# Kernel optimization log

Hardware: AMD Instinct MI355X
Metric: run time of the kernel (lower is better)

## Reference

```python
import jax, jax.numpy as jnp
import numpy as np

B, LQ, LK, D = 16, 1024, 4096, 256
SQRT_SCALE_INV = 0.25          # D ** -0.25, so scale = 1/sqrt(D)
HALF_BW = 128 // 2             # stripe_bandwdith // 2
NEG_INF = float('-inf')


def setup_inputs() -> dict:
    key = jax.random.key(0)
    k1, k2, k3, k4 = jax.random.split(key, 4)
    query = jax.random.normal(k1, (B, LQ, D), jnp.float32)
    key_t = jax.random.normal(k2, (B, LK, D), jnp.float32)
    value = jax.random.normal(k3, (B, LK, D), jnp.float32)
    # key lengths in [LK//2, LK]; masked_fill in torch requires max == LK
    key_lengths = jax.random.randint(k4, (B,), LK // 2, LK + 1).astype(jnp.int32)
    key_lengths = key_lengths.at[0].set(LK)
    query_lengths = jnp.full((B,), LQ, dtype=jnp.int32)  # full so no all-masked rows
    mask = jnp.arange(LK)[None, :] < key_lengths[:, None]  # [B, LK] bool, True = valid
    return {"query": query, "key": key_t, "value": value, "mask": mask,
            "query_lengths": query_lengths, "key_lengths": key_lengths}


def _stripe_mask(query_lengths, key_lengths, Lq, Lk):
    # band around line y = x * (key_len / query_len), per sample
    gx = jnp.arange(Lq, dtype=jnp.float32)[None, :, None]   # [1,Lq,1]
    gy = jnp.arange(Lk, dtype=jnp.float32)[None, None, :]   # [1,1,Lk]
    slope = (key_lengths.astype(jnp.float32) /
             query_lengths.astype(jnp.float32))[:, None, None]  # [B,1,1]
    center = gx * slope
    return (gy >= center - HALF_BW) & (gy <= center + HALF_BW)  # [B,Lq,Lk] bool


def reference(query, key, value, mask, query_lengths, key_lengths):
    # scores = (q * s) @ (k * s)^T  ==  (q @ k^T) * s^2
    scores = jnp.einsum('bqd,bkd->bqk', query, key) * (SQRT_SCALE_INV * SQRT_SCALE_INV)
    stripe = _stripe_mask(query_lengths, key_lengths, query.shape[1], key.shape[1])
    full_mask = mask[:, None, :] & stripe                    # padding AND stripe
    scores = jnp.where(full_mask, scores.astype(jnp.float32), NEG_INF)
    weight = jax.nn.softmax(scores, axis=-1).astype(query.dtype)
    # module applies no dropout (p=0) and returns (attn_weight, value)
    return (weight, value)
```

## Files before the change

### kernel.cpp

```cpp
#include <hip/hip_runtime.h>
#include <math.h>

constexpr int B_  = 16;
constexpr int LQ_ = 1024;
constexpr int LK_ = 4096;
constexpr int D_  = 256;
constexpr float HALF_BW_F = 64.0f;
constexpr float SCALE = 0.0625f;

typedef float fx4 __attribute__((ext_vector_type(4)));

constexpr int NB_PAD = 168;
constexpr int ROWS_PER_BLK = 16;
constexpr int NUNIT = (B_ * LQ_) / ROWS_PER_BLK;
constexpr int NXCD = 8;
constexpr int UNIT_PER_XCD = NUNIT / NXCD;

template <int CTRL>
__device__ __forceinline__ float dpp_add(float v) {
    int x = __builtin_amdgcn_update_dpp(0, __float_as_int(v), CTRL, 0xF, 0xF, true);
    return v + __int_as_float(x);
}
__device__ __forceinline__ float dpp_reduce16(float v) {
    v = dpp_add<0x118>(v); v = dpp_add<0x114>(v);
    v = dpp_add<0x112>(v); v = dpp_add<0x111>(v);
    return v;
}

__device__ __forceinline__ float grp16_max(float v) {
    #pragma unroll
    for (int off = 8; off > 0; off >>= 1)
        v = fmaxf(v, __shfl_xor(v, off, 64));
    return v;
}
__device__ __forceinline__ float grp16_sum(float v) {
    #pragma unroll
    for (int off = 8; off > 0; off >>= 1)
        v += __shfl_xor(v, off, 64);
    return v;
}

__global__ __launch_bounds__(256, 2) void stripe_attn_kernel(
    const float* __restrict__ Q, const float* __restrict__ K,
    const float* __restrict__ V,
    const int* __restrict__ qlen, const int* __restrict__ klen,
    float* __restrict__ Wout, float* __restrict__ Vout)
{
    const int Bid  = blockIdx.x;
    const int xcd  = Bid & 7;
    const int type = (Bid >> 3) & 1;
    const int rb   = xcd * UNIT_PER_XCD + (Bid >> 4);
    const int tid  = threadIdx.x;
    const int lane = tid & 63;
    const int wave = tid >> 6;
    const int row0 = rb * ROWS_PER_BLK + wave * 4;
    const int b    = row0 >> 10;
    const int qi0  = row0 & (LQ_ - 1);

    __shared__ float s_sc[4][4 * NB_PAD];

    const int   key_len = klen[b];
    const float slope   = (float)key_len / (float)qlen[b];

    int k_lo[4], k_hi[4];
    #pragma unroll
    for (int r = 0; r < 4; ++r) {
        const float center = (float)(qi0 + r) * slope;
        int lo = (int)ceilf(center - HALF_BW_F); if (lo < 0) lo = 0;
        int hi = (int)floorf(center + HALF_BW_F); if (hi > key_len - 1) hi = key_len - 1;
        k_lo[r] = lo; k_hi[r] = hi;
    }

    if (type == 1) {
        const float* vs = V    + (size_t)row0 * 1024;
        float*       vd = Vout + (size_t)row0 * 1024;
        #pragma unroll
        for (int it = 0; it < 16; ++it) {
            const int o = (it * 64 + lane) * 4;
            fx4 t = __builtin_nontemporal_load((const fx4*)(vs + o));
            __builtin_nontemporal_store(t, (fx4*)(vd + o));
        }
        const fx4 z4 = {0.f, 0.f, 0.f, 0.f};
        #pragma unroll
        for (int r = 0; r < 4; ++r) {
            const int s_lo = k_lo[r] >> 8, s_hi = k_hi[r] >> 8;
            float* base = Wout + (size_t)(row0 + r) * LK_;
            #pragma unroll
            for (int j = 0; j < 16; ++j) {
                if (j < s_lo || j > s_hi)
                    __builtin_nontemporal_store(z4, (fx4*)(base + (j * 64 + lane) * 4));
            }
        }
        return;
    }

    const int g   = lane >> 4;
    const int l   = lane & 15;
    const int lo0 = k_lo[0], hi3 = k_hi[3];

    const float* qbase = Q + ((size_t)b * LQ_ + qi0) * D_;
    float4 q0[4], q1[4], q2[4], q3[4];
    #pragma unroll
    for (int m = 0; m < 4; ++m) {
        q0[m] = *(const float4*)(qbase + 0 * D_ + l * 16 + m * 4);
        q1[m] = *(const float4*)(qbase + 1 * D_ + l * 16 + m * 4);
        q2[m] = *(const float4*)(qbase + 2 * D_ + l * 16 + m * 4);
        q3[m] = *(const float4*)(qbase + 3 * D_ + l * 16 + m * 4);
    }

    const float* kbase = K + (size_t)b * LK_ * D_;
    float* sw = s_sc[wave];
    #pragma unroll 2
    for (int kk0 = lo0; kk0 <= hi3; kk0 += 8) {
        const int keyA  = kk0 + g;
        const int keyB  = kk0 + g + 4;
        const int keyAc = (keyA <= hi3) ? keyA : hi3;
        const int keyBc = (keyB <= hi3) ? keyB : hi3;
        const float* kpA = kbase + (size_t)keyAc * D_ + l * 16;
        const float* kpB = kbase + (size_t)keyBc * D_ + l * 16;
        float4 kfA[4], kfB[4];
        #pragma unroll
        for (int m = 0; m < 4; ++m) kfA[m] = *(const float4*)(kpA + m * 4);
        #pragma unroll
        for (int m = 0; m < 4; ++m) kfB[m] = *(const float4*)(kpB + m * 4);
        float a0 = 0.f, a1 = 0.f, a2 = 0.f, a3 = 0.f;
        float b0 = 0.f, b1 = 0.f, b2 = 0.f, b3 = 0.f;
        #pragma unroll
        for (int m = 0; m < 4; ++m) {
            a0 += q0[m].x*kfA[m].x + q0[m].y*kfA[m].y + q0[m].z*kfA[m].z + q0[m].w*kfA[m].w;
            a1 += q1[m].x*kfA[m].x + q1[m].y*kfA[m].y + q1[m].z*kfA[m].z + q1[m].w*kfA[m].w;
            a2 += q2[m].x*kfA[m].x + q2[m].y*kfA[m].y + q2[m].z*kfA[m].z + q2[m].w*kfA[m].w;
            a3 += q3[m].x*kfA[m].x + q3[m].y*kfA[m].y + q3[m].z*kfA[m].z + q3[m].w*kfA[m].w;
            b0 += q0[m].x*kfB[m].x + q0[m].y*kfB[m].y + q0[m].z*kfB[m].z + q0[m].w*kfB[m].w;
            b1 += q1[m].x*kfB[m].x + q1[m].y*kfB[m].y + q1[m].z*kfB[m].z + q1[m].w*kfB[m].w;
            b2 += q2[m].x*kfB[m].x + q2[m].y*kfB[m].y + q2[m].z*kfB[m].z + q2[m].w*kfB[m].w;
            b3 += q3[m].x*kfB[m].x + q3[m].y*kfB[m].y + q3[m].z*kfB[m].z + q3[m].w*kfB[m].w;
        }
        a0 = dpp_reduce16(a0); a1 = dpp_reduce16(a1);
        a2 = dpp_reduce16(a2); a3 = dpp_reduce16(a3);
        b0 = dpp_reduce16(b0); b1 = dpp_reduce16(b1);
        b2 = dpp_reduce16(b2); b3 = dpp_reduce16(b3);
        if (l == 15) {
            if (keyA >= k_lo[0] && keyA <= k_hi[0]) sw[0*NB_PAD + keyA - k_lo[0]] = a0 * SCALE;
            if (keyA >= k_lo[1] && keyA <= k_hi[1]) sw[1*NB_PAD + keyA - k_lo[1]] = a1 * SCALE;
            if (keyA >= k_lo[2] && keyA <= k_hi[2]) sw[2*NB_PAD + keyA - k_lo[2]] = a2 * SCALE;
            if (keyA >= k_lo[3] && keyA <= k_hi[3]) sw[3*NB_PAD + keyA - k_lo[3]] = a3 * SCALE;
            if (keyB >= k_lo[0] && keyB <= k_hi[0]) sw[0*NB_PAD + keyB - k_lo[0]] = b0 * SCALE;
            if (keyB >= k_lo[1] && keyB <= k_hi[1]) sw[1*NB_PAD + keyB - k_lo[1]] = b1 * SCALE;
            if (keyB >= k_lo[2] && keyB <= k_hi[2]) sw[2*NB_PAD + keyB - k_lo[2]] = b2 * SCALE;
            if (keyB >= k_lo[3] && keyB <= k_hi[3]) sw[3*NB_PAD + keyB - k_lo[3]] = b3 * SCALE;
        }
    }

    const float center_g = (float)(qi0 + g) * slope;
    int klo_g = (int)ceilf(center_g - HALF_BW_F); if (klo_g < 0) klo_g = 0;
    int khi_g = (int)floorf(center_g + HALF_BW_F); if (khi_g > key_len - 1) khi_g = key_len - 1;
    const int nb_g = khi_g - klo_g + 1;
    float* sg = sw + g * NB_PAD;

    float vj[9];
    #pragma unroll
    for (int j = 0; j < 9; ++j) {
        const int idx = l + j * 16;
        vj[j] = (idx < nb_g) ? sg[idx] : -INFINITY;
    }
    float mx = vj[0];
    #pragma unroll
    for (int j = 1; j < 9; ++j) mx = fmaxf(mx, vj[j]);
    mx = grp16_max(mx);

    float ej[9], ssum = 0.f;
    #pragma unroll
    for (int j = 0; j < 9; ++j) { ej[j] = __expf(vj[j] - mx); ssum += ej[j]; }
    ssum = grp16_sum(ssum);
    const float inv = 1.0f / ssum;
    #pragma unroll
    for (int j = 0; j < 9; ++j)
        sg[l + j * 16] = ej[j] * inv;

    #pragma unroll
    for (int r = 0; r < 4; ++r) {
        const int klo = k_lo[r], khi = k_hi[r];
        const int s_lo = klo >> 8, s_hi = khi >> 8;
        float* base = Wout + (size_t)(row0 + r) * LK_;
        const float* sr = sw + r * NB_PAD;
        for (int j = s_lo; j <= s_hi; ++j) {
            const int c0 = (j * 64 + lane) * 4;
            float w[4] = {0.f, 0.f, 0.f, 0.f};
            if (c0 + 3 >= klo && c0 <= khi) {
                #pragma unroll
                for (int i = 0; i < 4; ++i) {
                    const int c = c0 + i;
                    if (c >= klo && c <= khi) w[i] = sr[c - klo];
                }
            }
            fx4 w4; w4.x = w[0]; w4.y = w[1]; w4.z = w[2]; w4.w = w[3];
            __builtin_nontemporal_store(w4, (fx4*)(base + c0));
        }
    }
}

extern "C" void kernel_launch(void* const* d_in, const int* in_sizes, int n_in,
                              void* d_out, int out_size, void* d_ws, size_t ws_size,
                              hipStream_t stream) {
    const float* Q    = (const float*)d_in[0];
    const float* K    = (const float*)d_in[1];
    const float* V    = (const float*)d_in[2];
    const int*   qlen = (const int*)d_in[4];
    const int*   klen = (const int*)d_in[5];

    float* Wout = (float*)d_out;
    const size_t W_ELEMS = (size_t)B_ * LQ_ * LK_;
    float* Vout = Wout + W_ELEMS;

    stripe_attn_kernel<<<dim3(2 * NUNIT), dim3(256), 0, stream>>>(
        Q, K, V, qlen, klen, Wout, Vout);
}
```

Before: 96.36 us.

## Share K tiles across waves via async global-to-LDS double-buffered staging

Each block now computes the union of the key bands of its 16 rows and streams those K rows into a double-buffered LDS tile with direct global-to-LDS loads. All four waves then read the shared tile instead of each wave loading its own overlapping K rows from global memory. The Q register layout is changed to match the LDS read pattern. This removes redundant K traffic across waves, but adds a block-wide barrier per 16-key chunk and more LDS, and waves spend cycles on chunks outside their own band.

```diff
diff --git a/kernel.cpp b/kernel.cpp
--- a/kernel.cpp
+++ b/kernel.cpp
@@ -15,6 +15,7 @@
 constexpr int NUNIT = (B_ * LQ_) / ROWS_PER_BLK;
 constexpr int NXCD = 8;
 constexpr int UNIT_PER_XCD = NUNIT / NXCD;
+constexpr int CHUNK = 16;
 
 template <int CTRL>
 __device__ __forceinline__ float dpp_add(float v) {
@@ -26,7 +27,6 @@
     v = dpp_add<0x112>(v); v = dpp_add<0x111>(v);
     return v;
 }
-
 __device__ __forceinline__ float grp16_max(float v) {
     #pragma unroll
     for (int off = 8; off > 0; off >>= 1)
@@ -38,6 +38,13 @@
     for (int off = 8; off > 0; off >>= 1)
         v += __shfl_xor(v, off, 64);
     return v;
+}
+
+__device__ __forceinline__ void gload16(const float* g, float* l) {
+    __builtin_amdgcn_global_load_lds(
+        (const __attribute__((address_space(1))) float*)g,
+        (__attribute__((address_space(3))) float*)l,
+        16, 0, 0);
 }
 
 __global__ __launch_bounds__(256, 2) void stripe_attn_kernel(
@@ -57,8 +64,6 @@
     const int b    = row0 >> 10;
     const int qi0  = row0 & (LQ_ - 1);
 
-    __shared__ float s_sc[4][4 * NB_PAD];
-
     const int   key_len = klen[b];
     const float slope   = (float)key_len / (float)qlen[b];
 
@@ -94,62 +99,94 @@
         return;
     }
 
+    __shared__ float kbuf[2][CHUNK * 256];
+    __shared__ float s_sc[4][4 * NB_PAD];
+
     const int g   = lane >> 4;
     const int l   = lane & 15;
     const int lo0 = k_lo[0], hi3 = k_hi[3];
 
-    const float* qbase = Q + ((size_t)b * LQ_ + qi0) * D_;
+    const int qi_blk = (rb * ROWS_PER_BLK) & (LQ_ - 1);
+    int lo_b = (int)ceilf((float)qi_blk * slope - HALF_BW_F);
+    if (lo_b < 0) lo_b = 0;
+    int hi_b = (int)floorf((float)(qi_blk + 15) * slope + HALF_BW_F);
+    if (hi_b > key_len - 1) hi_b = key_len - 1;
+    const int nchunks = (hi_b - lo_b + CHUNK) / CHUNK;
+
+    const float* qbase = Q + ((size_t)b * LQ_ + qi0) * D_ + l * 4;
     float4 q0[4], q1[4], q2[4], q3[4];
     #pragma unroll
     for (int m = 0; m < 4; ++m) {
-        q0[m] = *(const float4*)(qbase + 0 * D_ + l * 16 + m * 4);
-        q1[m] = *(const float4*)(qbase + 1 * D_ + l * 16 + m * 4);
-        q2[m] = *(const float4*)(qbase + 2 * D_ + l * 16 + m * 4);
-        q3[m] = *(const float4*)(qbase + 3 * D_ + l * 16 + m * 4);
+        q0[m] = *(const float4*)(qbase + 0 * D_ + m * 64);
+        q1[m] = *(const float4*)(qbase + 1 * D_ + m * 64);
+        q2[m] = *(const float4*)(qbase + 2 * D_ + m * 64);
+        q3[m] = *(const float4*)(qbase + 3 * D_ + m * 64);
     }
 
     const float* kbase = K + (size_t)b * LK_ * D_;
     float* sw = s_sc[wave];
-    #pragma unroll 2
-    for (int kk0 = lo0; kk0 <= hi3; kk0 += 8) {
-        const int keyA  = kk0 + g;
-        const int keyB  = kk0 + g + 4;
-        const int keyAc = (keyA <= hi3) ? keyA : hi3;
-        const int keyBc = (keyB <= hi3) ? keyB : hi3;
-        const float* kpA = kbase + (size_t)keyAc * D_ + l * 16;
-        const float* kpB = kbase + (size_t)keyBc * D_ + l * 16;
-        float4 kfA[4], kfB[4];
+
+    auto stage = [&](int c, int buf) {
+        const int base_key = lo_b + c * CHUNK + wave * 4;
         #pragma unroll
-        for (int m = 0; m < 4; ++m) kfA[m] = *(const float4*)(kpA + m * 4);
-        #pragma unroll
-        for (int m = 0; m < 4; ++m) kfB[m] = *(const float4*)(kpB + m * 4);
-        float a0 = 0.f, a1 = 0.f, a2 = 0.f, a3 = 0.f;
-        float b0 = 0.f, b1 = 0.f, b2 = 0.f, b3 = 0.f;
-        #pragma unroll
-        for (int m = 0; m < 4; ++m) {
-            a0 += q0[m].x*kfA[m].x + q0[m].y*kfA[m].y + q0[m].z*kfA[m].z + q0[m].w*kfA[m].w;
-            a1 += q1[m].x*kfA[m].x + q1[m].y*kfA[m].y + q1[m].z*kfA[m].z + q1[m].w*kfA[m].w;
-            a2 += q2[m].x*kfA[m].x + q2[m].y*kfA[m].y + q2[m].z*kfA[m].z + q2[m].w*kfA[m].w;
-            a3 += q3[m].x*kfA[m].x + q3[m].y*kfA[m].y + q3[m].z*kfA[m].z + q3[m].w*kfA[m].w;
-            b0 += q0[m].x*kfB[m].x + q0[m].y*kfB[m].y + q0[m].z*kfB[m].z + q0[m].w*kfB[m].w;
-            b1 += q1[m].x*kfB[m].x + q1[m].y*kfB[m].y + q1[m].z*kfB[m].z + q1[m].w*kfB[m].w;
-            b2 += q2[m].x*kfB[m].x + q2[m].y*kfB[m].y + q2[m].z*kfB[m].z + q2[m].w*kfB[m].w;
-            b3 += q3[m].x*kfB[m].x + q3[m].y*kfB[m].y + q3[m].z*kfB[m].z + q3[m].w*kfB[m].w;
-        }
-        a0 = dpp_reduce16(a0); a1 = dpp_reduce16(a1);
-        a2 = dpp_reduce16(a2); a3 = dpp_reduce16(a3);
-        b0 = dpp_reduce16(b0); b1 = dpp_reduce16(b1);
-        b2 = dpp_reduce16(b2); b3 = dpp_reduce16(b3);
-        if (l == 15) {
-            if (keyA >= k_lo[0] && keyA <= k_hi[0]) sw[0*NB_PAD + keyA - k_lo[0]] = a0 * SCALE;
-            if (keyA >= k_lo[1] && keyA <= k_hi[1]) sw[1*NB_PAD + keyA - k_lo[1]] = a1 * SCALE;
-            if (keyA >= k_lo[2] && keyA <= k_hi[2]) sw[2*NB_PAD + keyA - k_lo[2]] = a2 * SCALE;
-            if (keyA >= k_lo[3] && keyA <= k_hi[3]) sw[3*NB_PAD + keyA - k_lo[3]] = a3 * SCALE;
-            if (keyB >= k_lo[0] && keyB <= k_hi[0]) sw[0*NB_PAD + keyB - k_lo[0]] = b0 * SCALE;
-            if (keyB >= k_lo[1] && keyB <= k_hi[1]) sw[1*NB_PAD + keyB - k_lo[1]] = b1 * SCALE;
-            if (keyB >= k_lo[2] && keyB <= k_hi[2]) sw[2*NB_PAD + keyB - k_lo[2]] = b2 * SCALE;
-            if (keyB >= k_lo[3] && keyB <= k_hi[3]) sw[3*NB_PAD + keyB - k_lo[3]] = b3 * SCALE;
-        }
+        for (int s = 0; s < 4; ++s) {
+            int key = base_key + s;
+            if (key > hi_b) key = hi_b;
+            gload16(kbase + (size_t)key * D_ + lane * 4,
+                    &kbuf[buf][(wave * 4 + s) * 256]);
+        }
+    };
+
+    stage(0, 0);
+    __syncthreads();
+
+    for (int c = 0; c < nchunks; ++c) {
+        const int cb = c & 1;
+        if (c + 1 < nchunks) stage(c + 1, cb ^ 1);
+
+        const int cbase = lo_b + c * CHUNK;
+        if (cbase + CHUNK - 1 >= lo0 && cbase <= hi3) {
+            const float* kl = kbuf[cb];
+            #pragma unroll
+            for (int t = 0; t < 2; ++t) {
+                const int jA = g + 8 * t, jB = g + 4 + 8 * t;
+                const int keyA = cbase + jA, keyB = cbase + jB;
+                float4 kfA[4], kfB[4];
+                #pragma unroll
+                for (int m = 0; m < 4; ++m) {
+                    kfA[m] = *(const float4*)(kl + jA * 256 + m * 64 + l * 4);
+                    kfB[m] = *(const float4*)(kl + jB * 256 + m * 64 + l * 4);
+                }
+                float a0 = 0.f, a1 = 0.f, a2 = 0.f, a3 = 0.f;
+                float b0 = 0.f, b1 = 0.f, b2 = 0.f, b3 = 0.f;
+                #pragma unroll
+                for (int m = 0; m < 4; ++m) {
+                    a0 += q0[m].x*kfA[m].x + q0[m].y*kfA[m].y + q0[m].z*kfA[m].z + q0[m].w*kfA[m].w;
+                    a1 += q1[m].x*kfA[m].x + q1[m].y*kfA[m].y + q1[m].z*kfA[m].z + q1[m].w*kfA[m].w;
+                    a2 += q2[m].x*kfA[m].x + q2[m].y*kfA[m].y + q2[m].z*kfA[m].z + q2[m].w*kfA[m].w;
+                    a3 += q3[m].x*kfA[m].x + q3[m].y*kfA[m].y + q3[m].z*kfA[m].z + q3[m].w*kfA[m].w;
+                    b0 += q0[m].x*kfB[m].x + q0[m].y*kfB[m].y + q0[m].z*kfB[m].z + q0[m].w*kfB[m].w;
+                    b1 += q1[m].x*kfB[m].x + q1[m].y*kfB[m].y + q1[m].z*kfB[m].z + q1[m].w*kfB[m].w;
+                    b2 += q2[m].x*kfB[m].x + q2[m].y*kfB[m].y + q2[m].z*kfB[m].z + q2[m].w*kfB[m].w;
+                    b3 += q3[m].x*kfB[m].x + q3[m].y*kfB[m].y + q3[m].z*kfB[m].z + q3[m].w*kfB[m].w;
+                }
+                a0 = dpp_reduce16(a0); a1 = dpp_reduce16(a1);
+                a2 = dpp_reduce16(a2); a3 = dpp_reduce16(a3);
+                b0 = dpp_reduce16(b0); b1 = dpp_reduce16(b1);
+                b2 = dpp_reduce16(b2); b3 = dpp_reduce16(b3);
+                if (l == 15) {
+                    if (keyA >= k_lo[0] && keyA <= k_hi[0]) sw[0*NB_PAD + keyA - k_lo[0]] = a0 * SCALE;
+                    if (keyA >= k_lo[1] && keyA <= k_hi[1]) sw[1*NB_PAD + keyA - k_lo[1]] = a1 * SCALE;
+                    if (keyA >= k_lo[2] && keyA <= k_hi[2]) sw[2*NB_PAD + keyA - k_lo[2]] = a2 * SCALE;
+                    if (keyA >= k_lo[3] && keyA <= k_hi[3]) sw[3*NB_PAD + keyA - k_lo[3]] = a3 * SCALE;
+                    if (keyB >= k_lo[0] && keyB <= k_hi[0]) sw[0*NB_PAD + keyB - k_lo[0]] = b0 * SCALE;
+                    if (keyB >= k_lo[1] && keyB <= k_hi[1]) sw[1*NB_PAD + keyB - k_lo[1]] = b1 * SCALE;
+                    if (keyB >= k_lo[2] && keyB <= k_hi[2]) sw[2*NB_PAD + keyB - k_lo[2]] = b2 * SCALE;
+                    if (keyB >= k_lo[3] && keyB <= k_hi[3]) sw[3*NB_PAD + keyB - k_lo[3]] = b3 * SCALE;
+                }
+            }
+        }
+        __syncthreads();
     }
 
     const float center_g = (float)(qi0 + g) * slope;
```

Result: slower. 102.2 us (+6.1%).
